# Kernel optimization log

Hardware: AMD Instinct MI355X
Metric: run time of the kernel (lower is better)

Reference implementation:

```python
import jax, jax.numpy as jnp
from jax import lax
import numpy as np

D_MODEL = 512
D_INNER = 1024
DT_RANK = 32
D_STATE = 16
D_CONV = 3
B, L = 2, 1024
SQ = 4  # sqrt(d_state)


def setup_inputs() -> dict:
    key = jax.random.key(0)
    ks = jax.random.split(key, 16)
    s = lambda *sh: 1.0 / np.sqrt(sh[-1])
    inp = {
        "x": jax.random.normal(ks[0], (B, L, D_MODEL), jnp.float32),
        "h": jax.random.normal(ks[1], (B, L, D_INNER, D_STATE), jnp.float32),
        "in_proj_w": jax.random.normal(ks[2], (2 * D_INNER, D_MODEL), jnp.float32) * s(D_MODEL),
        "conv1d_w": jax.random.normal(ks[3], (D_INNER, 1, D_CONV), jnp.float32) * 0.3,
        "conv1d_b": jax.random.normal(ks[4], (D_INNER,), jnp.float32) * 0.02,
        "x_proj_w": jax.random.normal(ks[5], (DT_RANK + 2 * D_STATE, D_INNER), jnp.float32) * s(D_INNER),
        "dt_proj_w": jax.random.normal(ks[6], (D_INNER, DT_RANK), jnp.float32) * s(DT_RANK),
        "dt_proj_b": jax.random.normal(ks[7], (D_INNER,), jnp.float32) * 0.1 - 4.0,
        "A_log": jnp.log(jnp.tile(jnp.arange(1, D_STATE + 1, dtype=jnp.float32), (D_INNER, 1))),
        "D": jnp.ones((D_INNER,), jnp.float32),
        "sf1_w": jax.random.normal(ks[8], (D_INNER, 1, 1, 1), jnp.float32) * 0.3,
        "sf1_b": jax.random.normal(ks[9], (D_INNER,), jnp.float32) * 0.02,
        "sf2_w": jax.random.normal(ks[10], (D_INNER, 1, 3, 3), jnp.float32) * 0.3,
        "sf2_b": jax.random.normal(ks[11], (D_INNER,), jnp.float32) * 0.02,
        "alpha": jnp.ones((2,), jnp.float32),
        "out_proj_w": jax.random.normal(ks[12], (D_MODEL, D_INNER), jnp.float32) * s(D_INNER),
    }
    return inp


def _dwconv1d(x_bdl, w, b):
    # x: [B, D, L], w: [D, 1, K], groups=D, SAME padding (K=3, pad=1)
    y = lax.conv_general_dilated(x_bdl, w, (1,), [(1, 1)],
                                 dimension_numbers=("NCH", "OIH", "NCH"),
                                 feature_group_count=D_INNER)
    return y + b[None, :, None]


def _dwconv2d(x, w, b, pad):
    y = lax.conv_general_dilated(x, w, (1, 1), [(pad, pad), (pad, pad)],
                                 dimension_numbers=("NCHW", "OIHW", "NCHW"),
                                 feature_group_count=D_INNER)
    return y + b[None, :, None, None]


def reference(x, h, in_proj_w, conv1d_w, conv1d_b, x_proj_w, dt_proj_w, dt_proj_b,
              A_log, D, sf1_w, sf1_b, sf2_w, sf2_b, alpha, out_proj_w):
    # in_proj -> split x/z
    xz = x @ in_proj_w.T                       # [B, L, 2*Di]
    xc, z = jnp.split(xz, 2, axis=-1)
    # depthwise causal-ish conv1d over L
    xc = _dwconv1d(jnp.transpose(xc, (0, 2, 1)), conv1d_w, conv1d_b)
    xs = jax.nn.silu(jnp.transpose(xc, (0, 2, 1)))  # [B, L, Di]

    # ssm_step
    A = -jnp.exp(A_log)                         # [Di, S]
    dBC = xs @ x_proj_w.T                       # [B, L, R+2S]
    delta, Bm, Cm = jnp.split(dBC, [DT_RANK, DT_RANK + D_STATE], axis=-1)
    delta = jax.nn.softplus(delta @ dt_proj_w.T + dt_proj_b)  # [B, L, Di]
    deltaA = jnp.exp(delta[..., None] * A)      # [B, L, Di, S]
    BX = (delta * xs)[..., None] * Bm[:, :, None, :]
    hn = deltaA * h + BX                        # [B, L, Di, S]

    # state fusion: reshape state dim S into 4x4 spatial, depthwise 1x1 + 3x3 convs
    h2 = hn.reshape(B * L, D_INNER, SQ, SQ)
    hf = alpha[0] * _dwconv2d(h2, sf1_w, sf1_b, 0) + alpha[1] * _dwconv2d(h2, sf2_w, sf2_b, 1)
    hn = hf.reshape(B, L, D_INNER, D_STATE)

    y = jnp.einsum("blds,bls->bld", hn, Cm) + D * xs
    out = (y * jax.nn.silu(z)) @ out_proj_w.T   # [B, L, Dm]
    return out, hn
```

## Files before the change

### kernel.cpp

```cpp
#include <hip/hip_runtime.h>
#include <stdint.h>

#define BLT 2048
#define DMODEL 512
#define DINNER 1024
#define TCH 8

typedef __bf16 bf16x8 __attribute__((ext_vector_type(8)));
typedef float f32x4 __attribute__((ext_vector_type(4)));

__global__ __launch_bounds__(256) void gemm_mfma(const float* __restrict__ A,
                                                 const float* __restrict__ B,
                                                 float* __restrict__ C,
                                                 int M, int N, int K) {
    __shared__ __bf16 As[128][72];
    __shared__ __bf16 Bs[128][72];
    const int tid = threadIdx.x;
    const int wave = tid >> 6, lane = tid & 63;
    const int waveM = wave >> 1, waveN = wave & 1;
    const int quad = lane >> 4, l16 = lane & 15;
    const int m0 = blockIdx.y * 128, n0 = blockIdx.x * 128;

    f32x4 acc[4][4];
#pragma unroll
    for (int mi = 0; mi < 4; mi++)
#pragma unroll
        for (int ni = 0; ni < 4; ni++) acc[mi][ni] = (f32x4){0.f, 0.f, 0.f, 0.f};

    const int sr = tid >> 4;
    const int sc = (tid & 15) * 4;

    for (int k0 = 0; k0 < K; k0 += 64) {
#pragma unroll
        for (int p = 0; p < 8; p++) {
            int r = sr + p * 16;
            float4 v = *(const float4*)(A + (size_t)(m0 + r) * K + k0 + sc);
            union { __bf16 b[4]; uint2 u; } pk;
            pk.b[0] = (__bf16)v.x; pk.b[1] = (__bf16)v.y;
            pk.b[2] = (__bf16)v.z; pk.b[3] = (__bf16)v.w;
            *(uint2*)&As[r][sc] = pk.u;
        }
#pragma unroll
        for (int p = 0; p < 8; p++) {
            int r = sr + p * 16;
            float4 v = *(const float4*)(B + (size_t)(n0 + r) * K + k0 + sc);
            union { __bf16 b[4]; uint2 u; } pk;
            pk.b[0] = (__bf16)v.x; pk.b[1] = (__bf16)v.y;
            pk.b[2] = (__bf16)v.z; pk.b[3] = (__bf16)v.w;
            *(uint2*)&Bs[r][sc] = pk.u;
        }
        __syncthreads();
#pragma unroll
        for (int kk = 0; kk < 64; kk += 32) {
            bf16x8 af[4], bfr[4];
#pragma unroll
            for (int mi = 0; mi < 4; mi++)
                af[mi] = *(const bf16x8*)&As[waveM * 64 + mi * 16 + l16][kk + quad * 8];
#pragma unroll
            for (int ni = 0; ni < 4; ni++)
                bfr[ni] = *(const bf16x8*)&Bs[waveN * 64 + ni * 16 + l16][kk + quad * 8];
#pragma unroll
            for (int mi = 0; mi < 4; mi++)
#pragma unroll
                for (int ni = 0; ni < 4; ni++)
                    acc[mi][ni] = __builtin_amdgcn_mfma_f32_16x16x32_bf16(
                        af[mi], bfr[ni], acc[mi][ni], 0, 0, 0);
        }
        __syncthreads();
    }
#pragma unroll
    for (int mi = 0; mi < 4; mi++)
#pragma unroll
        for (int ni = 0; ni < 4; ni++)
#pragma unroll
            for (int reg = 0; reg < 4; reg++) {
                int m = m0 + waveM * 64 + mi * 16 + quad * 4 + reg;
                int n = n0 + waveN * 64 + ni * 16 + l16;
                C[(size_t)m * N + n] = acc[mi][ni][reg];
            }
}

__global__ __launch_bounds__(256) void gemm_mfma_64(const float* __restrict__ A,
                                                    const float* __restrict__ B,
                                                    float* __restrict__ C,
                                                    int M, int N, int K) {
    __shared__ __bf16 As[64][72];
    __shared__ __bf16 Bs[64][72];
    const int tid = threadIdx.x;
    const int wave = tid >> 6, lane = tid & 63;
    const int waveM = wave >> 1, waveN = wave & 1;
    const int quad = lane >> 4, l16 = lane & 15;
    const int m0 = blockIdx.y * 64, n0 = blockIdx.x * 64;

    f32x4 acc[2][2];
#pragma unroll
    for (int mi = 0; mi < 2; mi++)
#pragma unroll
        for (int ni = 0; ni < 2; ni++) acc[mi][ni] = (f32x4){0.f, 0.f, 0.f, 0.f};

    const int sr = tid >> 4;
    const int sc = (tid & 15) * 4;

    for (int k0 = 0; k0 < K; k0 += 64) {
#pragma unroll
        for (int p = 0; p < 4; p++) {
            int r = sr + p * 16;
            float4 v = *(const float4*)(A + (size_t)(m0 + r) * K + k0 + sc);
            union { __bf16 b[4]; uint2 u; } pk;
            pk.b[0] = (__bf16)v.x; pk.b[1] = (__bf16)v.y;
            pk.b[2] = (__bf16)v.z; pk.b[3] = (__bf16)v.w;
            *(uint2*)&As[r][sc] = pk.u;
        }
#pragma unroll
        for (int p = 0; p < 4; p++) {
            int r = sr + p * 16;
            float4 v = *(const float4*)(B + (size_t)(n0 + r) * K + k0 + sc);
            union { __bf16 b[4]; uint2 u; } pk;
            pk.b[0] = (__bf16)v.x; pk.b[1] = (__bf16)v.y;
            pk.b[2] = (__bf16)v.z; pk.b[3] = (__bf16)v.w;
            *(uint2*)&Bs[r][sc] = pk.u;
        }
        __syncthreads();
#pragma unroll
        for (int kk = 0; kk < 64; kk += 32) {
            bf16x8 af[2], bfr[2];
#pragma unroll
            for (int mi = 0; mi < 2; mi++)
                af[mi] = *(const bf16x8*)&As[waveM * 32 + mi * 16 + l16][kk + quad * 8];
#pragma unroll
            for (int ni = 0; ni < 2; ni++)
                bfr[ni] = *(const bf16x8*)&Bs[waveN * 32 + ni * 16 + l16][kk + quad * 8];
#pragma unroll
            for (int mi = 0; mi < 2; mi++)
#pragma unroll
                for (int ni = 0; ni < 2; ni++)
                    acc[mi][ni] = __builtin_amdgcn_mfma_f32_16x16x32_bf16(
                        af[mi], bfr[ni], acc[mi][ni], 0, 0, 0);
        }
        __syncthreads();
    }
#pragma unroll
    for (int mi = 0; mi < 2; mi++)
#pragma unroll
        for (int ni = 0; ni < 2; ni++)
#pragma unroll
            for (int reg = 0; reg < 4; reg++) {
                int m = m0 + waveM * 32 + mi * 16 + quad * 4 + reg;
                int n = n0 + waveN * 32 + ni * 16 + l16;
                C[(size_t)m * N + n] = acc[mi][ni][reg];
            }
}

__global__ __launch_bounds__(256) void gemm_mfma_s_splitk(const float* __restrict__ A,
                                                          const float* __restrict__ B,
                                                          float* __restrict__ Cpart,
                                                          int M, int N, int K, int kchunk) {
    __shared__ __bf16 As[32][72];
    __shared__ __bf16 Bs[64][72];
    const int tid = threadIdx.x;
    const int wave = tid >> 6, lane = tid & 63;
    const int waveM = wave >> 1, waveN = wave & 1;
    const int quad = lane >> 4, l16 = lane & 15;
    const int m0 = blockIdx.y * 32, n0 = blockIdx.x * 64;
    const int kbeg = blockIdx.z * kchunk;
    const int kend = kbeg + kchunk;

    f32x4 acc[2];
    acc[0] = (f32x4){0.f, 0.f, 0.f, 0.f};
    acc[1] = (f32x4){0.f, 0.f, 0.f, 0.f};

    const int sr = tid >> 4;
    const int sc = (tid & 15) * 4;

    for (int k0 = kbeg; k0 < kend; k0 += 64) {
#pragma unroll
        for (int p = 0; p < 2; p++) {
            int r = sr + p * 16;
            float4 v = *(const float4*)(A + (size_t)(m0 + r) * K + k0 + sc);
            union { __bf16 b[4]; uint2 u; } pk;
            pk.b[0] = (__bf16)v.x; pk.b[1] = (__bf16)v.y;
            pk.b[2] = (__bf16)v.z; pk.b[3] = (__bf16)v.w;
            *(uint2*)&As[r][sc] = pk.u;
        }
#pragma unroll
        for (int p = 0; p < 4; p++) {
            int r = sr + p * 16;
            float4 v = *(const float4*)(B + (size_t)(n0 + r) * K + k0 + sc);
            union { __bf16 b[4]; uint2 u; } pk;
            pk.b[0] = (__bf16)v.x; pk.b[1] = (__bf16)v.y;
            pk.b[2] = (__bf16)v.z; pk.b[3] = (__bf16)v.w;
            *(uint2*)&Bs[r][sc] = pk.u;
        }
        __syncthreads();
#pragma unroll
        for (int kk = 0; kk < 64; kk += 32) {
            bf16x8 af = *(const bf16x8*)&As[waveM * 16 + l16][kk + quad * 8];
#pragma unroll
            for (int ni = 0; ni < 2; ni++) {
                bf16x8 bf = *(const bf16x8*)&Bs[waveN * 32 + ni * 16 + l16][kk + quad * 8];
                acc[ni] = __builtin_amdgcn_mfma_f32_16x16x32_bf16(af, bf, acc[ni], 0, 0, 0);
            }
        }
        __syncthreads();
    }
    float* Cz = Cpart + (size_t)blockIdx.z * M * N;
#pragma unroll
    for (int ni = 0; ni < 2; ni++)
#pragma unroll
        for (int reg = 0; reg < 4; reg++) {
            int m = m0 + waveM * 16 + quad * 4 + reg;
            int n = n0 + waveN * 32 + ni * 16 + l16;
            Cz[(size_t)m * N + n] = acc[ni][reg];
        }
}

__global__ __launch_bounds__(256) void prep_k(const float* __restrict__ dtw,
                                              const float* __restrict__ A_log,
                                              float* __restrict__ dtwT,
                                              float* __restrict__ Aneg) {
    int i = blockIdx.x * 256 + threadIdx.x;
    {
        int r = i >> 10, d = i & 1023;
        dtwT[i] = dtw[d * 32 + r];
    }
    if (i < 16384) Aneg[i] = -__expf(A_log[i]);
}

__global__ __launch_bounds__(256) void conv1d_silu_k(const float* __restrict__ xz,
                                                     const float* __restrict__ w,
                                                     const float* __restrict__ bias,
                                                     float* __restrict__ xs) {
    int idx = blockIdx.x * 256 + threadIdx.x;
    int t = idx >> 10, d = idx & 1023;
    int l = t & 1023;
    float cur = xz[(size_t)t * 2048 + d];
    float prev = (l > 0) ? xz[(size_t)(t - 1) * 2048 + d] : 0.f;
    float nxt = (l < 1023) ? xz[(size_t)(t + 1) * 2048 + d] : 0.f;
    float v = w[d * 3] * prev + w[d * 3 + 1] * cur + w[d * 3 + 2] * nxt + bias[d];
    xs[idx] = v / (1.f + __expf(-v));
}

__global__ __launch_bounds__(256) void ssm_fuse_k(
    const float* __restrict__ h,
    const float* __restrict__ xz,
    const float* __restrict__ xs,
    const float* __restrict__ dBCp,
    const float* __restrict__ dtwT,
    const float* __restrict__ dtb,
    const float* __restrict__ Aneg,
    const float* __restrict__ Dp,
    const float* __restrict__ sf1w, const float* __restrict__ sf1b,
    const float* __restrict__ sf2w, const float* __restrict__ sf2b,
    const float* __restrict__ alpha,
    float* __restrict__ hn_out,
    float* __restrict__ yz) {
    const int tid = threadIdx.x;
    const int d = blockIdx.x * 256 + tid;
    const int t0 = blockIdx.y * TCH;

    __shared__ float dbc_s[TCH * 64];
    {
        const size_t base = (size_t)t0 * 64;
        const size_t st = (size_t)BLT * 64;
#pragma unroll
        for (int i = tid; i < TCH * 64; i += 256) {
            const size_t o = base + i;
            dbc_s[i] = dBCp[o] + dBCp[o + st] + dBCp[o + 2 * st] + dBCp[o + 3 * st];
        }
    }
    __syncthreads();

    float dtw_r[32];
#pragma unroll
    for (int r = 0; r < 32; r++) dtw_r[r] = dtwT[r * 1024 + d];
    float an[16];
    {
        const float4* apv = (const float4*)(Aneg + (size_t)d * 16);
#pragma unroll
        for (int q = 0; q < 4; q++) {
            float4 aq = apv[q];
            an[q * 4 + 0] = aq.x; an[q * 4 + 1] = aq.y;
            an[q * 4 + 2] = aq.z; an[q * 4 + 3] = aq.w;
        }
    }
    float w2[9];
#pragma unroll
    for (int k = 0; k < 9; k++) w2[k] = sf2w[d * 9 + k];
    const float w1 = sf1w[d], b1 = sf1b[d], b2v = sf2b[d];
    const float a0f = alpha[0], a1f = alpha[1];
    const float dtb_d = dtb[d], Dp_d = Dp[d];

#pragma unroll
    for (int tt = 0; tt < TCH; tt++) {
        const int t = t0 + tt;
        const size_t td = (size_t)t * 1024 + d;
        const float xv = xs[td];
        const float zv = xz[(size_t)t * 2048 + 1024 + d];
        float hv[16];
        {
            const float4* hp = (const float4*)(h + td * 16);
#pragma unroll
            for (int q = 0; q < 4; q++) {
                float4 hq = hp[q];
                hv[q * 4 + 0] = hq.x; hv[q * 4 + 1] = hq.y;
                hv[q * 4 + 2] = hq.z; hv[q * 4 + 3] = hq.w;
            }
        }
        float accd = dtb_d;
#pragma unroll
        for (int r = 0; r < 32; r++) accd += dbc_s[tt * 64 + r] * dtw_r[r];
        const float dt = (accd > 20.f) ? accd : __logf(1.f + __expf(accd));
        const float dx = dt * xv;

        float hn[16];
#pragma unroll
        for (int s = 0; s < 16; s++)
            hn[s] = __expf(dt * an[s]) * hv[s] + dx * dbc_s[tt * 64 + 32 + s];

        float hf[16];
#pragma unroll
        for (int i = 0; i < 4; i++)
#pragma unroll
            for (int j = 0; j < 4; j++) {
                float s2 = b2v;
#pragma unroll
                for (int ki = 0; ki < 3; ki++)
#pragma unroll
                    for (int kj = 0; kj < 3; kj++) {
                        int ii = i + ki - 1, jj = j + kj - 1;
                        if (ii >= 0 && ii < 4 && jj >= 0 && jj < 4)
                            s2 += hn[ii * 4 + jj] * w2[ki * 3 + kj];
                    }
                hf[i * 4 + j] = a0f * (w1 * hn[i * 4 + j] + b1) + a1f * s2;
            }
        float y = Dp_d * xv;
#pragma unroll
        for (int s = 0; s < 16; s++) y += hf[s] * dbc_s[tt * 64 + 48 + s];
        yz[td] = y * (zv / (1.f + __expf(-zv)));
        f32x4* op = (f32x4*)(hn_out + td * 16);
#pragma unroll
        for (int q = 0; q < 4; q++) {
            f32x4 v4 = (f32x4){hf[q * 4 + 0], hf[q * 4 + 1], hf[q * 4 + 2], hf[q * 4 + 3]};
            __builtin_nontemporal_store(v4, op + q);
        }
    }
}

extern "C" void kernel_launch(void* const* d_in, const int* in_sizes, int n_in,
                              void* d_out, int out_size, void* d_ws, size_t ws_size,
                              hipStream_t stream) {
    const float* x         = (const float*)d_in[0];
    const float* h         = (const float*)d_in[1];
    const float* in_proj_w = (const float*)d_in[2];
    const float* conv1d_w  = (const float*)d_in[3];
    const float* conv1d_b  = (const float*)d_in[4];
    const float* x_proj_w  = (const float*)d_in[5];
    const float* dt_proj_w = (const float*)d_in[6];
    const float* dt_proj_b = (const float*)d_in[7];
    const float* A_log     = (const float*)d_in[8];
    const float* Dp        = (const float*)d_in[9];
    const float* sf1w      = (const float*)d_in[10];
    const float* sf1b      = (const float*)d_in[11];
    const float* sf2w      = (const float*)d_in[12];
    const float* sf2b      = (const float*)d_in[13];
    const float* alpha     = (const float*)d_in[14];
    const float* out_projw = (const float*)d_in[15];

    float* out0   = (float*)d_out;
    float* hn_out = out0 + (size_t)BLT * DMODEL;

    float* xz   = (float*)d_ws;
    float* xs   = xz + (size_t)BLT * 2048;
    float* dBCp = xs + (size_t)BLT * DINNER;
    float* yz   = dBCp + (size_t)4 * BLT * 64;
    float* dtwT = yz + (size_t)BLT * DINNER;
    float* Aneg = dtwT + 32 * 1024;

    prep_k<<<128, 256, 0, stream>>>(dt_proj_w, A_log, dtwT, Aneg);
    gemm_mfma_64<<<dim3(2048 / 64, BLT / 64), 256, 0, stream>>>(x, in_proj_w, xz,
                                                                BLT, 2048, DMODEL);
    conv1d_silu_k<<<(BLT * DINNER) / 256, 256, 0, stream>>>(xz, conv1d_w, conv1d_b, xs);
    gemm_mfma_s_splitk<<<dim3(1, BLT / 32, 4), 256, 0, stream>>>(xs, x_proj_w, dBCp,
                                                                 BLT, 64, DINNER, 256);
    ssm_fuse_k<<<dim3(4, BLT / TCH), 256, 0, stream>>>(h, xz, xs, dBCp, dtwT, dt_proj_b,
                                                       Aneg, Dp, sf1w, sf1b, sf2w, sf2b, alpha,
                                                       hn_out, yz);
    gemm_mfma_64<<<dim3(DMODEL / 64, BLT / 64), 256, 0, stream>>>(yz, out_projw, out0,
                                                                  BLT, DMODEL, DINNER);
}
```

Baseline: 459.9 us.

## Shrink SSM time chunk, swizzle GEMM blocks, use regular stores for state

Lowers the per-block time chunk of the SSM kernel from 8 to 2 steps, which raises block count and parallelism but cuts per-block reuse of the weights loaded into registers. The small GEMM kernel gets an XCD-aware block-index swizzle so neighbouring tiles land on the same chiplet. hn output stores switch from nontemporal to ordinary stores, and the unused 128-tile GEMM kernel is deleted. The mix of changes may help or hurt depending on whether the SSM kernel was occupancy-limited or bound by register-reload overhead.

```diff
diff --git a/kernel.cpp b/kernel.cpp
--- a/kernel.cpp
+++ b/kernel.cpp
@@ -4,81 +4,10 @@
 #define BLT 2048
 #define DMODEL 512
 #define DINNER 1024
-#define TCH 8
+#define TCH 2
 
 typedef __bf16 bf16x8 __attribute__((ext_vector_type(8)));
 typedef float f32x4 __attribute__((ext_vector_type(4)));
-
-__global__ __launch_bounds__(256) void gemm_mfma(const float* __restrict__ A,
-                                                 const float* __restrict__ B,
-                                                 float* __restrict__ C,
-                                                 int M, int N, int K) {
-    __shared__ __bf16 As[128][72];
-    __shared__ __bf16 Bs[128][72];
-    const int tid = threadIdx.x;
-    const int wave = tid >> 6, lane = tid & 63;
-    const int waveM = wave >> 1, waveN = wave & 1;
-    const int quad = lane >> 4, l16 = lane & 15;
-    const int m0 = blockIdx.y * 128, n0 = blockIdx.x * 128;
-
-    f32x4 acc[4][4];
-#pragma unroll
-    for (int mi = 0; mi < 4; mi++)
-#pragma unroll
-        for (int ni = 0; ni < 4; ni++) acc[mi][ni] = (f32x4){0.f, 0.f, 0.f, 0.f};
-
-    const int sr = tid >> 4;
-    const int sc = (tid & 15) * 4;
-
-    for (int k0 = 0; k0 < K; k0 += 64) {
-#pragma unroll
-        for (int p = 0; p < 8; p++) {
-            int r = sr + p * 16;
-            float4 v = *(const float4*)(A + (size_t)(m0 + r) * K + k0 + sc);
-            union { __bf16 b[4]; uint2 u; } pk;
-            pk.b[0] = (__bf16)v.x; pk.b[1] = (__bf16)v.y;
-            pk.b[2] = (__bf16)v.z; pk.b[3] = (__bf16)v.w;
-            *(uint2*)&As[r][sc] = pk.u;
-        }
-#pragma unroll
-        for (int p = 0; p < 8; p++) {
-            int r = sr + p * 16;
-            float4 v = *(const float4*)(B + (size_t)(n0 + r) * K + k0 + sc);
-            union { __bf16 b[4]; uint2 u; } pk;
-            pk.b[0] = (__bf16)v.x; pk.b[1] = (__bf16)v.y;
-            pk.b[2] = (__bf16)v.z; pk.b[3] = (__bf16)v.w;
-            *(uint2*)&Bs[r][sc] = pk.u;
-        }
-        __syncthreads();
-#pragma unroll
-        for (int kk = 0; kk < 64; kk += 32) {
-            bf16x8 af[4], bfr[4];
-#pragma unroll
-            for (int mi = 0; mi < 4; mi++)
-                af[mi] = *(const bf16x8*)&As[waveM * 64 + mi * 16 + l16][kk + quad * 8];
-#pragma unroll
-            for (int ni = 0; ni < 4; ni++)
-                bfr[ni] = *(const bf16x8*)&Bs[waveN * 64 + ni * 16 + l16][kk + quad * 8];
-#pragma unroll
-            for (int mi = 0; mi < 4; mi++)
-#pragma unroll
-                for (int ni = 0; ni < 4; ni++)
-                    acc[mi][ni] = __builtin_amdgcn_mfma_f32_16x16x32_bf16(
-                        af[mi], bfr[ni], acc[mi][ni], 0, 0, 0);
-        }
-        __syncthreads();
-    }
-#pragma unroll
-    for (int mi = 0; mi < 4; mi++)
-#pragma unroll
-        for (int ni = 0; ni < 4; ni++)
-#pragma unroll
-            for (int reg = 0; reg < 4; reg++) {
-                int m = m0 + waveM * 64 + mi * 16 + quad * 4 + reg;
-                int n = n0 + waveN * 64 + ni * 16 + l16;
-                C[(size_t)m * N + n] = acc[mi][ni][reg];
-            }
-}
 
 __global__ __launch_bounds__(256) void gemm_mfma_64(const float* __restrict__ A,
                                                     const float* __restrict__ B,
@@ -90,7 +19,13 @@
     const int wave = tid >> 6, lane = tid & 63;
     const int waveM = wave >> 1, waveN = wave & 1;
     const int quad = lane >> 4, l16 = lane & 15;
-    const int m0 = blockIdx.y * 64, n0 = blockIdx.x * 64;
+
+    const int nwg = gridDim.x * gridDim.y;
+    const int bid = blockIdx.y * gridDim.x + blockIdx.x;
+    const int cpx = nwg >> 3;
+    const int swz = (bid & 7) * cpx + (bid >> 3);
+    const int bx = swz % gridDim.x, by = swz / gridDim.x;
+    const int m0 = by * 64, n0 = bx * 64;
 
     f32x4 acc[2][2];
 #pragma unroll
@@ -259,14 +194,10 @@
     const int t0 = blockIdx.y * TCH;
 
     __shared__ float dbc_s[TCH * 64];
-    {
-        const size_t base = (size_t)t0 * 64;
+    if (tid < TCH * 64) {
+        const size_t o = (size_t)t0 * 64 + tid;
         const size_t st = (size_t)BLT * 64;
-#pragma unroll
-        for (int i = tid; i < TCH * 64; i += 256) {
-            const size_t o = base + i;
-            dbc_s[i] = dBCp[o] + dBCp[o + st] + dBCp[o + 2 * st] + dBCp[o + 3 * st];
-        }
+        dbc_s[tid] = dBCp[o] + dBCp[o + st] + dBCp[o + 2 * st] + dBCp[o + 3 * st];
     }
     __syncthreads();
 
@@ -337,12 +268,10 @@
 #pragma unroll
         for (int s = 0; s < 16; s++) y += hf[s] * dbc_s[tt * 64 + 48 + s];
         yz[td] = y * (zv / (1.f + __expf(-zv)));
-        f32x4* op = (f32x4*)(hn_out + td * 16);
-#pragma unroll
-        for (int q = 0; q < 4; q++) {
-            f32x4 v4 = (f32x4){hf[q * 4 + 0], hf[q * 4 + 1], hf[q * 4 + 2], hf[q * 4 + 3]};
-            __builtin_nontemporal_store(v4, op + q);
-        }
+        float4* op = (float4*)(hn_out + td * 16);
+#pragma unroll
+        for (int q = 0; q < 4; q++)
+            op[q] = make_float4(hf[q * 4 + 0], hf[q * 4 + 1], hf[q * 4 + 2], hf[q * 4 + 3]);
     }
 }
 
```

Measured after the change: 397.0 us. -13.7%, faster.
